# Kernel tuning notes

Hardware: AMD Instinct MI355X
Metric: run time of the kernel (lower is better)

Reference implementation:

```python
import jax, jax.numpy as jnp
import numpy as np

IN_FEATURES = 8192
OUT_FEATURES = 28672


def setup_inputs() -> dict:
    key = jax.random.key(0)
    k1, k2, k3 = jax.random.split(key, 3)
    inputs = jax.random.normal(k1, (16, 1, IN_FEATURES), dtype=jnp.float32)
    # int8 quantized weight (stored as int8, values in [-127, 127])
    weight = jax.random.randint(k2, (OUT_FEATURES, IN_FEATURES), -127, 128, dtype=jnp.int8)
    # per-output-channel dequant scale
    weight_scaler = jax.random.uniform(k3, (OUT_FEATURES,), dtype=jnp.float32) * 0.01 + 1e-4
    return {"inputs": inputs, "weight": weight, "weight_scaler": weight_scaler}


def reference(inputs, weight, weight_scaler):
    # F.linear(inputs, weight): [..., in] @ [out, in]^T -> [..., out]
    # int8 weight is promoted to the activation dtype for the matmul,
    # then the per-channel scale is applied to the output.
    w = weight.astype(inputs.dtype)
    out = jnp.einsum('bsi,oi->bso', inputs, w)  # [B, S, out]
    return out * weight_scaler  # broadcast over last (out-channel) dim
```

## Files before the change

### kernel.cpp

```cpp
#include <hip/hip_runtime.h>
#include <hip/hip_bf16.h>
#include <stdint.h>


using f32x4 = __attribute__((ext_vector_type(4))) float;
using s16x8 = __attribute__((ext_vector_type(8))) short;
using i32x4 = __attribute__((ext_vector_type(4))) int;

static constexpr int K      = 8192;
static constexpr int N      = 28672;
static constexpr int NSTEPS = K / 32;
static constexpr int WK     = 256;
static constexpr int KSPLIT = 4;
static constexpr int KRANGE = K / KSPLIT;
static constexpr int NWIN   = KRANGE / WK;
static constexpr int SPW    = WK / 32;

__global__ __launch_bounds__(256) void prep_a_kernel(const float* __restrict__ act,
                                                     uint4* __restrict__ afrag) {
  const int t   = blockIdx.x * 256 + threadIdx.x;
  const int kk  = t >> 6;
  const int l   = t & 63;
  const int row = l & 15;
  const int q   = l >> 4;
  const float* src = act + row * K + kk * 32 + q * 8;
  uint d[4];
#pragma unroll
  for (int p = 0; p < 4; ++p) {
    uint u0 = __builtin_bit_cast(uint, src[2 * p]);
    uint u1 = __builtin_bit_cast(uint, src[2 * p + 1]);
    u0 += 0x7fffu + ((u0 >> 16) & 1u);
    u1 += 0x7fffu + ((u1 >> 16) & 1u);
    d[p] = (u0 >> 16) | (u1 & 0xffff0000u);
  }
  afrag[t] = make_uint4(d[0], d[1], d[2], d[3]);
}

__device__ __forceinline__ uint pack_bf16(int a, int b) {
  uint fa = __builtin_bit_cast(uint, (float)a);
  uint fb = __builtin_bit_cast(uint, (float)b);
  return (fa >> 16) | (fb & 0xffff0000u);
}

__global__ __launch_bounds__(64) void wq_linear_kernel(
    const int* __restrict__ wt,
    const uint4* __restrict__ afrag,
    const float* __restrict__ scaler,
    float* __restrict__ out) {
  __shared__ int buf[2][16 * WK];
  const int l  = threadIdx.x;
  const int c  = l & 15;
  const int q  = l >> 4;
  const int n0 = blockIdx.x << 4;
  const int kb = blockIdx.y * KRANGE;
  const int step0 = kb >> 5;

#define STAGE(mm, bi)                                                        \
  _Pragma("unroll") for (int r = 0; r < 16; ++r) {                           \
    const int sp = ((r & 3) << 1) | ((r >> 2) & 1);                          \
    const int* gsrc = wt + (size_t)(n0 + r) * K + kb + (mm) * WK             \
                      + ((l ^ sp) << 2);                                     \
    __builtin_amdgcn_global_load_lds(                                        \
        (const __attribute__((address_space(1))) unsigned int*)gsrc,         \
        (__attribute__((address_space(3))) unsigned int*)&buf[bi][r * WK],   \
        16, 0, 0);                                                           \
  }

  STAGE(0, 0)

  f32x4 acc = {0.f, 0.f, 0.f, 0.f};
  const int spc = ((c & 3) << 1) | ((c >> 2) & 1);

#pragma unroll 1
  for (int m = 0; m < NWIN; ++m) {
    uint4 ag[SPW];
#pragma unroll
    for (int s = 0; s < SPW; ++s)
      ag[s] = afrag[(size_t)(step0 + m * SPW + s) * 64 + l];

    if (m + 1 < NWIN) {
      STAGE(m + 1, (m + 1) & 1)
      asm volatile("s_waitcnt vmcnt(16)" ::: "memory");
    } else {
      asm volatile("s_waitcnt vmcnt(0)" ::: "memory");
    }
    __builtin_amdgcn_sched_barrier(0);

    const char* rowp = (const char*)&buf[m & 1][c * WK];
#pragma unroll
    for (int s = 0; s < SPW; ++s) {
      const int o0 = (s << 7) + (((q << 5) | 0)  ^ (spc << 4));
      const int o1 = (s << 7) + (((q << 5) | 16) ^ (spc << 4));
      const i32x4 w0 = *(const i32x4*)(rowp + o0);
      const i32x4 w1 = *(const i32x4*)(rowp + o1);
      const uint b0 = pack_bf16(w0.x, w0.y);
      const uint b1 = pack_bf16(w0.z, w0.w);
      const uint b2 = pack_bf16(w1.x, w1.y);
      const uint b3 = pack_bf16(w1.z, w1.w);
      s16x8 a = __builtin_bit_cast(s16x8, ag[s]);
      s16x8 b = __builtin_bit_cast(s16x8, make_uint4(b0, b1, b2, b3));
      acc = __builtin_amdgcn_mfma_f32_16x16x32_bf16(a, b, acc, 0, 0, 0);
    }
  }

  const float scl = scaler[n0 + c];
#pragma unroll
  for (int i = 0; i < 4; ++i) {
    const int b = (q << 2) + i;
    unsafeAtomicAdd(&out[(size_t)b * N + n0 + c], acc[i] * scl);
  }
#undef STAGE
}

extern "C" void kernel_launch(void* const* d_in, const int* in_sizes, int n_in,
                              void* d_out, int out_size, void* d_ws, size_t ws_size,
                              hipStream_t stream) {
  const float* act    = (const float*)d_in[0];
  const int*   wt     = (const int*)d_in[1];
  const float* scaler = (const float*)d_in[2];
  float*       out    = (float*)d_out;
  uint4*       afrag  = (uint4*)d_ws;

  hipMemsetAsync(out, 0, (size_t)out_size * sizeof(float), stream);
  prep_a_kernel<<<(NSTEPS * 64) / 256, 256, 0, stream>>>(act, afrag);
  dim3 grid(N / 16, KSPLIT);
  wq_linear_kernel<<<grid, 64, 0, stream>>>(wt, afrag, scaler, out);
}
```

Before: 193.3 us.

## Drop split-K atomics, widen K window to 512 with direct output stores

Removes the 4-way split over K, so each 64-thread block now covers the full K range for its 16 output columns and writes results with plain stores. This drops the output memset and the atomic adds. To keep more bytes in flight per block, the staged window doubles to 512 K-elements using two async global-to-LDS loads per row, and the wait count is raised to match. The grid shrinks to 1792 single-wave blocks, which may leave too little parallelism to saturate HBM bandwidth on a large GPU.

```diff
diff --git a/kernel.cpp b/kernel.cpp
--- a/kernel.cpp
+++ b/kernel.cpp
@@ -10,10 +10,8 @@
 static constexpr int K      = 8192;
 static constexpr int N      = 28672;
 static constexpr int NSTEPS = K / 32;
-static constexpr int WK     = 256;
-static constexpr int KSPLIT = 4;
-static constexpr int KRANGE = K / KSPLIT;
-static constexpr int NWIN   = KRANGE / WK;
+static constexpr int WK     = 512;
+static constexpr int NWIN   = K / WK;
 static constexpr int SPW    = WK / 32;
 
 __global__ __launch_bounds__(256) void prep_a_kernel(const float* __restrict__ act,
@@ -52,18 +50,19 @@
   const int c  = l & 15;
   const int q  = l >> 4;
   const int n0 = blockIdx.x << 4;
-  const int kb = blockIdx.y * KRANGE;
-  const int step0 = kb >> 5;
 
 #define STAGE(mm, bi)                                                        \
   _Pragma("unroll") for (int r = 0; r < 16; ++r) {                           \
     const int sp = ((r & 3) << 1) | ((r >> 2) & 1);                          \
-    const int* gsrc = wt + (size_t)(n0 + r) * K + kb + (mm) * WK             \
-                      + ((l ^ sp) << 2);                                     \
-    __builtin_amdgcn_global_load_lds(                                        \
-        (const __attribute__((address_space(1))) unsigned int*)gsrc,         \
-        (__attribute__((address_space(3))) unsigned int*)&buf[bi][r * WK],   \
-        16, 0, 0);                                                           \
+    _Pragma("unroll") for (int h = 0; h < 2; ++h) {                          \
+      const int* gsrc = wt + (size_t)(n0 + r) * K + (mm) * WK                \
+                        + ((((h << 6) + l) ^ sp) << 2);                      \
+      __builtin_amdgcn_global_load_lds(                                      \
+          (const __attribute__((address_space(1))) unsigned int*)gsrc,       \
+          (__attribute__((address_space(3))) unsigned int*)                  \
+              &buf[bi][r * WK + (h << 8)],                                   \
+          16, 0, 0);                                                         \
+    }                                                                        \
   }
 
   STAGE(0, 0)
@@ -76,11 +75,11 @@
     uint4 ag[SPW];
 #pragma unroll
     for (int s = 0; s < SPW; ++s)
-      ag[s] = afrag[(size_t)(step0 + m * SPW + s) * 64 + l];
+      ag[s] = afrag[(size_t)(m * SPW + s) * 64 + l];
 
     if (m + 1 < NWIN) {
       STAGE(m + 1, (m + 1) & 1)
-      asm volatile("s_waitcnt vmcnt(16)" ::: "memory");
+      asm volatile("s_waitcnt vmcnt(32)" ::: "memory");
     } else {
       asm volatile("s_waitcnt vmcnt(0)" ::: "memory");
     }
@@ -89,8 +88,8 @@
     const char* rowp = (const char*)&buf[m & 1][c * WK];
 #pragma unroll
     for (int s = 0; s < SPW; ++s) {
-      const int o0 = (s << 7) + (((q << 5) | 0)  ^ (spc << 4));
-      const int o1 = (s << 7) + (((q << 5) | 16) ^ (spc << 4));
+      const int o0 = (s << 7) + ((((q << 1) | 0) ^ spc) << 4);
+      const int o1 = (s << 7) + ((((q << 1) | 1) ^ spc) << 4);
       const i32x4 w0 = *(const i32x4*)(rowp + o0);
       const i32x4 w1 = *(const i32x4*)(rowp + o1);
       const uint b0 = pack_bf16(w0.x, w0.y);
@@ -105,10 +104,8 @@
 
   const float scl = scaler[n0 + c];
 #pragma unroll
-  for (int i = 0; i < 4; ++i) {
-    const int b = (q << 2) + i;
-    unsafeAtomicAdd(&out[(size_t)b * N + n0 + c], acc[i] * scl);
-  }
+  for (int i = 0; i < 4; ++i)
+    out[(size_t)((q << 2) + i) * N + n0 + c] = acc[i] * scl;
 #undef STAGE
 }
 
@@ -121,8 +118,6 @@
   float*       out    = (float*)d_out;
   uint4*       afrag  = (uint4*)d_ws;
 
-  hipMemsetAsync(out, 0, (size_t)out_size * sizeof(float), stream);
   prep_a_kernel<<<(NSTEPS * 64) / 256, 256, 0, stream>>>(act, afrag);
-  dim3 grid(N / 16, KSPLIT);
-  wq_linear_kernel<<<grid, 64, 0, stream>>>(wt, afrag, scaler, out);
+  wq_linear_kernel<<<N / 16, 64, 0, stream>>>(wt, afrag, scaler, out);
 }
```

After: 215.1 us. +11.2%, slower.
